# Kernel tuning notes

Hardware: AMD Instinct MI355X
Metric: run time of the kernel (lower is better)

Reference implementation:

```python
import jax, jax.numpy as jnp
import numpy as np

N_NODES = 200000
N_EDGES = 3200000
N_FEAT = 128
N_GRAPHS = 1000
N_CLASSES = 10
K = 30          # sort-pool k
C_CAT = 97      # 32+32+32+1 concatenated channels


def _glorot(k, shape):
    fan = shape[0] + shape[-1]
    return jax.random.normal(k, shape, jnp.float32) * (2.0 / fan) ** 0.5


def setup_inputs() -> dict:
    key = jax.random.key(0)
    ks = jax.random.split(key, 20)
    x = jax.random.normal(ks[0], (N_NODES, N_FEAT), jnp.float32)
    edge_index = jax.random.randint(ks[1], (2, N_EDGES), 0, N_NODES, jnp.int32)
    batch = jnp.sort(jax.random.randint(ks[2], (N_NODES,), 0, N_GRAPHS, jnp.int32))
    params = dict(
        W1=_glorot(ks[3], (N_FEAT, 32)), b1=jnp.zeros((32,), jnp.float32),
        W2=_glorot(ks[4], (32, 32)),     b2=jnp.zeros((32,), jnp.float32),
        W3=_glorot(ks[5], (32, 32)),     b3=jnp.zeros((32,), jnp.float32),
        W4=_glorot(ks[6], (32, 1)),      b4=jnp.zeros((1,), jnp.float32),
        conv5_w=_glorot(ks[7], (16, 1, 97)),  conv5_b=jnp.zeros((16,), jnp.float32),
        conv6_w=_glorot(ks[8], (32, 16, 5)),  conv6_b=jnp.zeros((32,), jnp.float32),
        fc1_w=_glorot(ks[9], (352, 128)),     fc1_b=jnp.zeros((128,), jnp.float32),
        fc2_w=_glorot(ks[10], (128, N_CLASSES)), fc2_b=jnp.zeros((N_CLASSES,), jnp.float32),
    )
    return dict(x=x, edge_index=edge_index, batch=batch, **params)


def reference(x, edge_index, batch, W1, b1, W2, b2, W3, b3, W4, b4,
              conv5_w, conv5_b, conv6_w, conv6_b, fc1_w, fc1_b, fc2_w, fc2_b):
    N = x.shape[0]
    src, dst = edge_index[0], edge_index[1]
    emask = (src != dst).astype(x.dtype)            # remove_self_loops
    deg = jax.ops.segment_sum(emask, dst, num_segments=N) + 1.0  # +1 for added self-loop
    inv_sqrt = jax.lax.rsqrt(deg)
    coef = emask * inv_sqrt[src] * inv_sqrt[dst]    # D^-1/2 (A) D^-1/2 edge weight
    inv_deg = 1.0 / deg                             # self-loop weight

    def gcn(h, W, b):
        hw = h @ W
        agg = jax.ops.segment_sum(hw[src] * coef[:, None], dst, num_segments=N)
        return agg + hw * inv_deg[:, None] + b

    x1 = jnp.tanh(gcn(x, W1, b1))
    x2 = jnp.tanh(gcn(x1, W2, b2))
    x3 = jnp.tanh(gcn(x2, W3, b3))
    x4 = jnp.tanh(gcn(x3, W4, b4))
    xc = jnp.concatenate([x1, x2, x3, x4], axis=-1)  # [N, 97]

    # SortAggregation(k=30): per-graph descending sort by last channel, top-k, zero pad
    perm = jnp.lexsort((-xc[:, -1], batch))          # batch-major, last channel desc
    xs, bs = xc[perm], batch[perm]
    counts = jax.ops.segment_sum(jnp.ones_like(batch), batch, num_segments=N_GRAPHS)
    starts = jnp.cumsum(counts) - counts
    rank = jnp.arange(N, dtype=jnp.int32) - starts[bs]
    valid = rank < K
    pooled = jnp.zeros((N_GRAPHS, K, C_CAT), xc.dtype).at[
        bs, jnp.where(valid, rank, K - 1)].add(jnp.where(valid[:, None], xs, 0.0))

    z = pooled.reshape(N_GRAPHS, 1, K * C_CAT)       # [G, 1, 2910]
    dn = ('NCH', 'OIH', 'NCH')
    z = jax.lax.conv_general_dilated(z, conv5_w, (97,), 'VALID', dimension_numbers=dn)
    z = jax.nn.relu(z + conv5_b[None, :, None])      # [G, 16, 30]
    z = jax.lax.reduce_window(z, -jnp.inf, jax.lax.max, (1, 1, 2), (1, 1, 2), 'VALID')
    z = jax.lax.conv_general_dilated(z, conv6_w, (1,), 'VALID', dimension_numbers=dn)
    z = jax.nn.relu(z + conv6_b[None, :, None])      # [G, 32, 11]
    z = z.reshape(N_GRAPHS, -1)                      # [G, 352]
    h = jax.nn.relu(z @ fc1_w + fc1_b)               # dropout is identity in eval
    return jax.nn.log_softmax(h @ fc2_w + fc2_b, axis=-1)
```

## Files before the change

kernel.cpp:

```cpp
#include <hip/hip_runtime.h>
#include <math.h>

#define NN 200000
#define NE 3200000
#define NF 128
#define NG 1000
#define KSEL 30
#define CCAT 97
#define NPAD 200704
#define SCAN_BLKS 196
#define EPADCAP (NE + 8 * NN)

#define BWID 512
#define NB 391
#define BCAP 10240
#define P1_CHUNK 8192
#define P1_BLKS 391

__global__ void k_p1_partition(const int* __restrict__ ei, int* __restrict__ bcursor,
                               int* __restrict__ ebuf) {
    __shared__ int lhist[NB];
    __shared__ int lbase[NB];
    int tid = threadIdx.x;
    int base = blockIdx.x * P1_CHUNK;
    for (int b = tid; b < NB; b += 256) lhist[b] = 0;
    __syncthreads();
    for (int it = 0; it < P1_CHUNK / 256; it++) {
        int e = base + it * 256 + tid;
        if (e < NE) {
            int s = ei[e], d = ei[NE + e];
            if (s != d) atomicAdd(&lhist[d >> 9], 1);
        }
    }
    __syncthreads();
    for (int b = tid; b < NB; b += 256) {
        int cnt = lhist[b];
        lbase[b] = cnt ? atomicAdd(&bcursor[b], cnt) : 0;
        lhist[b] = 0;
    }
    __syncthreads();
    for (int it = 0; it < P1_CHUNK / 256; it++) {
        int e = base + it * 256 + tid;
        if (e < NE) {
            int s = ei[e], d = ei[NE + e];
            if (s != d) {
                int b = d >> 9;
                int r = atomicAdd(&lhist[b], 1);
                int pos = lbase[b] + r;
                if (pos >= BCAP) pos = BCAP - 1;
                ebuf[b * BCAP + pos] = s | ((d & 511) << 18);
            }
        }
    }
}

__global__ void k_p2_count(const int* __restrict__ bcursor, const int* __restrict__ ebuf,
                           int* __restrict__ rowcnt, float* __restrict__ inv_sqrt) {
    __shared__ int lcnt[BWID];
    int b = blockIdx.x;
    int tid = threadIdx.x;
    for (int i = tid; i < BWID; i += 256) lcnt[i] = 0;
    __syncthreads();
    int size = bcursor[b];
    if (size > BCAP) size = BCAP;
    const int* eb = ebuf + b * BCAP;
    for (int k = tid; k < size; k += 256) atomicAdd(&lcnt[eb[k] >> 18], 1);
    __syncthreads();
    int node0 = b * BWID;
    for (int i = tid; i < BWID; i += 256) {
        int node = node0 + i;
        if (node < NN) {
            int c = lcnt[i];
            rowcnt[node] = (c + 7) & ~7;
            inv_sqrt[node] = rsqrtf((float)(c + 1));
        }
    }
}

__global__ void k_scanA(const int* __restrict__ in, int* __restrict__ out,
                        int* __restrict__ bsums) {
    __shared__ int s[1024];
    int tid = threadIdx.x;
    int gid = blockIdx.x * 1024 + tid;
    int v = in[gid];
    s[tid] = v;
    __syncthreads();
    for (int off = 1; off < 1024; off <<= 1) {
        int a = (tid >= off) ? s[tid - off] : 0;
        int cur = s[tid];
        __syncthreads();
        s[tid] = cur + a;
        __syncthreads();
    }
    out[gid] = s[tid] - v;
    if (tid == 1023) bsums[blockIdx.x] = s[tid];
}

__global__ void k_scanB(int* __restrict__ bsums) {
    __shared__ int s[256];
    int tid = threadIdx.x;
    int v = (tid < SCAN_BLKS) ? bsums[tid] : 0;
    s[tid] = v;
    __syncthreads();
    for (int off = 1; off < 256; off <<= 1) {
        int a = (tid >= off) ? s[tid - off] : 0;
        int cur = s[tid];
        __syncthreads();
        s[tid] = cur + a;
        __syncthreads();
    }
    if (tid < SCAN_BLKS) bsums[tid] = s[tid] - v;
}

__global__ void k_scanC(int* __restrict__ out, const int* __restrict__ bsums) {
    int gid = blockIdx.x * 1024 + threadIdx.x;
    out[gid] += bsums[blockIdx.x];
}

__global__ void k_p3_scatter(const int* __restrict__ bcursor, const int* __restrict__ ebuf,
                             const int* __restrict__ rowstart, int* __restrict__ esrc) {
    __shared__ int lcur[BWID];
    int b = blockIdx.x;
    int tid = threadIdx.x;
    int node0 = b * BWID;
    for (int i = tid; i < BWID; i += 256) lcur[i] = rowstart[node0 + i];
    __syncthreads();
    int size = bcursor[b];
    if (size > BCAP) size = BCAP;
    const int* eb = ebuf + b * BCAP;
    for (int k = tid; k < size; k += 256) {
        int v = eb[k];
        int local = v >> 18;
        int pos = atomicAdd(&lcur[local], 1);
        esrc[pos] = v & 0x3FFFF;
    }
    __syncthreads();
    for (int i = tid; i < BWID; i += 256) {
        int node = node0 + i;
        if (node < NN) {
            int end = rowstart[node + 1];
            for (int p = lcur[i]; p < end; p++) esrc[p] = NN;
        }
    }
}

template <int K>
__global__ void __launch_bounds__(256, 3) k_mm(const float* __restrict__ X,
                                               const float* __restrict__ W,
                                               const float* __restrict__ inv_sqrt,
                                               float* __restrict__ Y) {
    constexpr int K4 = K / 4;
    constexpr int RS = K4 + 1;
    __shared__ float4 sW[K * 8];
    __shared__ float4 sX[64 * RS];
    int tid = threadIdx.x;
    for (int i = tid; i < K * 8; i += 256) sW[i] = ((const float4*)W)[i];
    const float4* __restrict__ Xg = (const float4*)(X + (size_t)blockIdx.x * 64 * K);
    for (int i = tid; i < 64 * K4; i += 256) {
        int row = i / K4;
        int col = i & (K4 - 1);
        sX[row * RS + col] = Xg[i];
    }
    __syncthreads();
    int g = tid >> 3;
    int q = tid & 7;
    int r0 = blockIdx.x * 64 + g * 2;
    const float4* __restrict__ xr0 = &sX[(size_t)(g * 2 + 0) * RS];
    const float4* __restrict__ xr1 = &sX[(size_t)(g * 2 + 1) * RS];
    float4 a0 = make_float4(0.f, 0.f, 0.f, 0.f);
    float4 a1 = make_float4(0.f, 0.f, 0.f, 0.f);
#pragma unroll 4
    for (int k4 = 0; k4 < K4; k4++) {
        float4 x0 = xr0[k4];
        float4 x1 = xr1[k4];
        const float4* wk = &sW[k4 * 32 + q];
#pragma unroll
        for (int kk = 0; kk < 4; kk++) {
            float4 w = wk[kk * 8];
            float s0 = (kk == 0) ? x0.x : (kk == 1) ? x0.y : (kk == 2) ? x0.z : x0.w;
            float s1 = (kk == 0) ? x1.x : (kk == 1) ? x1.y : (kk == 2) ? x1.z : x1.w;
            a0.x = fmaf(s0, w.x, a0.x); a0.y = fmaf(s0, w.y, a0.y);
            a0.z = fmaf(s0, w.z, a0.z); a0.w = fmaf(s0, w.w, a0.w);
            a1.x = fmaf(s1, w.x, a1.x); a1.y = fmaf(s1, w.y, a1.y);
            a1.z = fmaf(s1, w.z, a1.z); a1.w = fmaf(s1, w.w, a1.w);
        }
    }
    float s0 = inv_sqrt[r0 + 0];
    float s1 = inv_sqrt[r0 + 1];
    a0.x *= s0; a0.y *= s0; a0.z *= s0; a0.w *= s0;
    a1.x *= s1; a1.y *= s1; a1.z *= s1; a1.w *= s1;
    ((float4*)(Y + (size_t)(r0 + 0) * 32))[q] = a0;
    ((float4*)(Y + (size_t)(r0 + 1) * 32))[q] = a1;
}

__global__ void k_aggr(const int* __restrict__ rowstart, const int* __restrict__ esrc,
                       const float* __restrict__ hws, const float* __restrict__ inv_sqrt,
                       const float* __restrict__ b, float* __restrict__ xout) {
    int t = blockIdx.x * 256 + threadIdx.x;
    int n = t >> 5, c = t & 31;
    if (n >= NN) return;
    int e0 = rowstart[n], e1 = rowstart[n + 1];
    float a[8];
    a[0] = hws[(size_t)n * 32 + c];
#pragma unroll
    for (int k = 1; k < 8; k++) a[k] = 0.0f;
    for (int e = e0; e < e1; e += 8) {
        int4 sA = *(const int4*)(esrc + e);
        int4 sB = *(const int4*)(esrc + e + 4);
        float v0 = hws[(size_t)sA.x * 32 + c];
        float v1 = hws[(size_t)sA.y * 32 + c];
        float v2 = hws[(size_t)sA.z * 32 + c];
        float v3 = hws[(size_t)sA.w * 32 + c];
        float v4 = hws[(size_t)sB.x * 32 + c];
        float v5 = hws[(size_t)sB.y * 32 + c];
        float v6 = hws[(size_t)sB.z * 32 + c];
        float v7 = hws[(size_t)sB.w * 32 + c];
        a[0] += v0; a[1] += v1; a[2] += v2; a[3] += v3;
        a[4] += v4; a[5] += v5; a[6] += v6; a[7] += v7;
    }
    float acc = ((a[0] + a[1]) + (a[2] + a[3])) + ((a[4] + a[5]) + (a[6] + a[7]));
    xout[t] = tanhf(fmaf(acc, inv_sqrt[n], b[c]));
}

__global__ void k_mm4(const float* __restrict__ x3, const float* __restrict__ W4,
                      const float* __restrict__ inv_sqrt, float* __restrict__ hws4) {
    int n = blockIdx.x * 256 + threadIdx.x;
    if (n >= NN) return;
    if (n == 0) hws4[NN] = 0.0f;
    const float4* xr = (const float4*)(x3 + (size_t)n * 32);
    float acc = 0.0f;
#pragma unroll
    for (int q = 0; q < 8; q++) {
        float4 v = xr[q];
        acc = fmaf(v.x, W4[q * 4 + 0], acc);
        acc = fmaf(v.y, W4[q * 4 + 1], acc);
        acc = fmaf(v.z, W4[q * 4 + 2], acc);
        acc = fmaf(v.w, W4[q * 4 + 3], acc);
    }
    hws4[n] = acc * inv_sqrt[n];
}

__global__ void k_aggr1(const int* __restrict__ rowstart, const int* __restrict__ esrc,
                        const float* __restrict__ hws4, const float* __restrict__ inv_sqrt,
                        const float* __restrict__ b4, float* __restrict__ x4) {
    int n = blockIdx.x * 256 + threadIdx.x;
    if (n >= NN) return;
    int e0 = rowstart[n], e1 = rowstart[n + 1];
    float a[8];
    a[0] = hws4[n];
#pragma unroll
    for (int k = 1; k < 8; k++) a[k] = 0.0f;
    for (int e = e0; e < e1; e += 8) {
        int4 sA = *(const int4*)(esrc + e);
        int4 sB = *(const int4*)(esrc + e + 4);
        a[0] += hws4[sA.x]; a[1] += hws4[sA.y];
        a[2] += hws4[sA.z]; a[3] += hws4[sA.w];
        a[4] += hws4[sB.x]; a[5] += hws4[sB.y];
        a[6] += hws4[sB.z]; a[7] += hws4[sB.w];
    }
    float acc = ((a[0] + a[1]) + (a[2] + a[3])) + ((a[4] + a[5]) + (a[6] + a[7]));
    x4[n] = tanhf(fmaf(acc, inv_sqrt[n], b4[0]));
}

__global__ void k_gbounds(const int* __restrict__ batch, int* __restrict__ starts) {
    int n = blockIdx.x * 256 + threadIdx.x;
    if (n >= NN) return;
    int bn = batch[n];
    int bp = (n == 0) ? -1 : batch[n - 1];
    for (int g = bp + 1; g <= bn; g++) starts[g] = n;
    if (n == NN - 1)
        for (int g = bn + 1; g <= NG; g++) starts[g] = NN;
}

__global__ void k_sortpool(const int* __restrict__ starts,
                           const float* __restrict__ x1, const float* __restrict__ x2,
                           const float* __restrict__ x3, const float* __restrict__ x4,
                           float* __restrict__ pooled) {
    __shared__ float keys[1024];
    __shared__ int sel[KSEL];
    int g = blockIdx.x;
    int tid = threadIdx.x;
    int start = starts[g];
    int cnt = starts[g + 1] - start;
    if (cnt > 1024) cnt = 1024;
    for (int i = tid; i < cnt; i += 256) keys[i] = x4[start + i];
    __syncthreads();
    for (int i = tid; i < cnt; i += 256) {
        float ki = keys[i];
        int rank = 0;
        for (int j = 0; j < cnt; j++) {
            float kj = keys[j];
            rank += (kj > ki) || (kj == ki && j < i);
        }
        if (rank < KSEL) sel[rank] = start + i;
    }
    __syncthreads();
    int selcnt = cnt < KSEL ? cnt : KSEL;
    for (int t = tid; t < KSEL * CCAT; t += 256) {
        int r = t / CCAT, ch = t - r * CCAT;
        float v = 0.0f;
        if (r < selcnt) {
            int node = sel[r];
            if (ch < 32)      v = x1[(size_t)node * 32 + ch];
            else if (ch < 64) v = x2[(size_t)node * 32 + ch - 32];
            else if (ch < 96) v = x3[(size_t)node * 32 + ch - 64];
            else              v = x4[node];
        }
        pooled[g * (KSEL * CCAT) + t] = v;
    }
}

__global__ void k_head(const float* __restrict__ pooled,
                       const float* __restrict__ w5, const float* __restrict__ b5,
                       const float* __restrict__ w6, const float* __restrict__ b6,
                       const float* __restrict__ fw1, const float* __restrict__ fb1,
                       const float* __restrict__ fw2, const float* __restrict__ fb2,
                       float* __restrict__ out) {
    __shared__ float sP[KSEL * CCAT];
    __shared__ float s5[16 * 30];
    __shared__ float smp[16 * 15];
    __shared__ float sz[352];
    __shared__ float sh[128];
    __shared__ float sl[10];
    int g = blockIdx.x;
    int tid = threadIdx.x;
    for (int i = tid; i < KSEL * CCAT; i += 256) sP[i] = pooled[g * (KSEL * CCAT) + i];
    __syncthreads();
    for (int t = tid; t < 16 * 30; t += 256) {
        int c = t / 30, j = t - c * 30;
        float acc = b5[c];
        for (int i = 0; i < CCAT; i++) acc = fmaf(sP[j * CCAT + i], w5[c * CCAT + i], acc);
        s5[c * 30 + j] = fmaxf(acc, 0.0f);
    }
    __syncthreads();
    for (int t = tid; t < 16 * 15; t += 256) {
        int c = t / 15, j = t - c * 15;
        smp[t] = fmaxf(s5[c * 30 + 2 * j], s5[c * 30 + 2 * j + 1]);
    }
    __syncthreads();
    for (int t = tid; t < 32 * 11; t += 256) {
        int c = t / 11, j = t - c * 11;
        float acc = b6[c];
        for (int ci = 0; ci < 16; ci++) {
#pragma unroll
            for (int k = 0; k < 5; k++)
                acc = fmaf(smp[ci * 15 + j + k], w6[(c * 16 + ci) * 5 + k], acc);
        }
        sz[t] = fmaxf(acc, 0.0f);
    }
    __syncthreads();
    if (tid < 128) {
        float acc = fb1[tid];
        for (int i = 0; i < 352; i++) acc = fmaf(sz[i], fw1[i * 128 + tid], acc);
        sh[tid] = fmaxf(acc, 0.0f);
    }
    __syncthreads();
    if (tid < 10) {
        float acc = fb2[tid];
        for (int i = 0; i < 128; i++) acc = fmaf(sh[i], fw2[i * 10 + tid], acc);
        sl[tid] = acc;
    }
    __syncthreads();
    if (tid < 10) {
        float m = -1e30f;
        for (int i = 0; i < 10; i++) m = fmaxf(m, sl[i]);
        float ssum = 0.0f;
        for (int i = 0; i < 10; i++) ssum += expf(sl[i] - m);
        out[g * 10 + tid] = sl[tid] - m - logf(ssum);
    }
}

extern "C" void kernel_launch(void* const* d_in, const int* in_sizes, int n_in,
                              void* d_out, int out_size, void* d_ws, size_t ws_size,
                              hipStream_t stream) {
    const float* x   = (const float*)d_in[0];
    const int*   ei  = (const int*)d_in[1];
    const int*   bat = (const int*)d_in[2];
    const float* W1  = (const float*)d_in[3];
    const float* b1  = (const float*)d_in[4];
    const float* W2  = (const float*)d_in[5];
    const float* b2  = (const float*)d_in[6];
    const float* W3  = (const float*)d_in[7];
    const float* b3  = (const float*)d_in[8];
    const float* W4  = (const float*)d_in[9];
    const float* b4  = (const float*)d_in[10];
    const float* w5  = (const float*)d_in[11];
    const float* b5  = (const float*)d_in[12];
    const float* w6  = (const float*)d_in[13];
    const float* b6  = (const float*)d_in[14];
    const float* fw1 = (const float*)d_in[15];
    const float* fb1 = (const float*)d_in[16];
    const float* fw2 = (const float*)d_in[17];
    const float* fb2 = (const float*)d_in[18];
    float* out = (float*)d_out;

    float* ws = (float*)d_ws;
    float* inv_sqrt = ws;
    float* hws      = inv_sqrt + NN;
    float* x1       = hws + (size_t)(NN + 1) * 32;
    float* x2       = x1 + (size_t)NN * 32;
    float* x3       = x2 + (size_t)NN * 32;
    float* x4       = x3 + (size_t)NN * 32;
    float* pooled   = x4 + NN;
    int* rowcnt     = (int*)(pooled + NG * KSEL * CCAT);
    int* rowstart   = rowcnt + NPAD;
    int* esrc       = rowstart + NPAD;
    int* bcursor    = esrc + EPADCAP;
    int* bsums      = bcursor + 512;
    int* gstarts    = bsums + 256;
    int* ebuf       = (int*)x3;

    const int TB = 256;
    int gN  = (NN + TB - 1) / TB;
    int gNC = (NN * 32 + TB - 1) / TB;
    int gMM = NN / 64;

    hipMemsetAsync(bcursor, 0, 512 * sizeof(int), stream);
    hipMemsetAsync(rowcnt, 0, NPAD * sizeof(int), stream);
    hipMemsetAsync(hws + (size_t)NN * 32, 0, 32 * sizeof(float), stream);
    k_p1_partition<<<P1_BLKS, TB, 0, stream>>>(ei, bcursor, ebuf);
    k_p2_count<<<NB, TB, 0, stream>>>(bcursor, ebuf, rowcnt, inv_sqrt);
    k_scanA<<<SCAN_BLKS, 1024, 0, stream>>>(rowcnt, rowstart, bsums);
    k_scanB<<<1, 256, 0, stream>>>(bsums);
    k_scanC<<<SCAN_BLKS, 1024, 0, stream>>>(rowstart, bsums);
    k_p3_scatter<<<NB, TB, 0, stream>>>(bcursor, ebuf, rowstart, esrc);

    k_gbounds<<<gN, TB, 0, stream>>>(bat, gstarts);

    k_mm<128><<<gMM, TB, 0, stream>>>(x, W1, inv_sqrt, hws);
    k_aggr<<<gNC, TB, 0, stream>>>(rowstart, esrc, hws, inv_sqrt, b1, x1);
    k_mm<32><<<gMM, TB, 0, stream>>>(x1, W2, inv_sqrt, hws);
    k_aggr<<<gNC, TB, 0, stream>>>(rowstart, esrc, hws, inv_sqrt, b2, x2);
    k_mm<32><<<gMM, TB, 0, stream>>>(x2, W3, inv_sqrt, hws);
    k_aggr<<<gNC, TB, 0, stream>>>(rowstart, esrc, hws, inv_sqrt, b3, x3);
    k_mm4<<<gN, TB, 0, stream>>>(x3, W4, inv_sqrt, hws);
    k_aggr1<<<gN, TB, 0, stream>>>(rowstart, esrc, hws, inv_sqrt, b4, x4);

    k_sortpool<<<NG, TB, 0, stream>>>(gstarts, x1, x2, x3, x4, pooled);
    k_head<<<NG, TB, 0, stream>>>(pooled, w5, b5, w6, b6, fw1, fb1, fw2, fb2, out);
}
```

Before: 585.6 us.

## Fuse next-layer matmul into aggregation epilogue and merge sortpool with head

The GCN aggregation kernel now computes the next layer's dense projection (32x32 or 32x1) in its epilogue, using shared memory for the row and a warp-shuffle reduction for the single-column case. Ping-pong hws buffers remove the separate k_mm and k_mm4 launches and their re-reads of x1/x2/x3. Sort-pool and the conv/FC head are merged into one kernel so the pooled tensor stays in shared memory instead of going through global memory. In exchange, each aggregation thread holds a 32-float weight column, which raises register pressure, and the aggregation kernel gains a block barrier.

```diff
diff --git a/kernel.cpp b/kernel.cpp
--- a/kernel.cpp
+++ b/kernel.cpp
@@ -193,12 +193,14 @@
     ((float4*)(Y + (size_t)(r0 + 1) * 32))[q] = a1;
 }
 
-__global__ void k_aggr(const int* __restrict__ rowstart, const int* __restrict__ esrc,
-                       const float* __restrict__ hws, const float* __restrict__ inv_sqrt,
-                       const float* __restrict__ b, float* __restrict__ xout) {
+template <int MODE>
+__global__ void k_aggr_f(const int* __restrict__ rowstart, const int* __restrict__ esrc,
+                         const float* __restrict__ hws, const float* __restrict__ inv_sqrt,
+                         const float* __restrict__ bvec, const float* __restrict__ Wn,
+                         float* __restrict__ xout, float* __restrict__ hnext) {
+    __shared__ float sxr[8][32];
     int t = blockIdx.x * 256 + threadIdx.x;
     int n = t >> 5, c = t & 31;
-    if (n >= NN) return;
     int e0 = rowstart[n], e1 = rowstart[n + 1];
     float a[8];
     a[0] = hws[(size_t)n * 32 + c];
@@ -219,25 +221,37 @@
         a[4] += v4; a[5] += v5; a[6] += v6; a[7] += v7;
     }
     float acc = ((a[0] + a[1]) + (a[2] + a[3])) + ((a[4] + a[5]) + (a[6] + a[7]));
-    xout[t] = tanhf(fmaf(acc, inv_sqrt[n], b[c]));
-}
-
-__global__ void k_mm4(const float* __restrict__ x3, const float* __restrict__ W4,
-                      const float* __restrict__ inv_sqrt, float* __restrict__ hws4) {
-    int n = blockIdx.x * 256 + threadIdx.x;
-    if (n >= NN) return;
-    if (n == 0) hws4[NN] = 0.0f;
-    const float4* xr = (const float4*)(x3 + (size_t)n * 32);
-    float acc = 0.0f;
-#pragma unroll
-    for (int q = 0; q < 8; q++) {
-        float4 v = xr[q];
-        acc = fmaf(v.x, W4[q * 4 + 0], acc);
-        acc = fmaf(v.y, W4[q * 4 + 1], acc);
-        acc = fmaf(v.z, W4[q * 4 + 2], acc);
-        acc = fmaf(v.w, W4[q * 4 + 3], acc);
-    }
-    hws4[n] = acc * inv_sqrt[n];
+    float invs = inv_sqrt[n];
+    float r = tanhf(fmaf(acc, invs, bvec[c]));
+    xout[t] = r;
+    if (MODE == 1) {
+        int ln = threadIdx.x >> 5;
+        sxr[ln][c] = r;
+        float wcol[32];
+#pragma unroll
+        for (int k = 0; k < 32; k++) wcol[k] = Wn[k * 32 + c];
+        __syncthreads();
+        const float4* xr = (const float4*)sxr[ln];
+        float h = 0.f;
+#pragma unroll
+        for (int j = 0; j < 8; j++) {
+            float4 xq = xr[j];
+            h = fmaf(xq.x, wcol[4 * j + 0], h);
+            h = fmaf(xq.y, wcol[4 * j + 1], h);
+            h = fmaf(xq.z, wcol[4 * j + 2], h);
+            h = fmaf(xq.w, wcol[4 * j + 3], h);
+        }
+        hnext[t] = h * invs;
+    } else {
+        float v = r * Wn[c];
+        v += __shfl_xor(v, 1);
+        v += __shfl_xor(v, 2);
+        v += __shfl_xor(v, 4);
+        v += __shfl_xor(v, 8);
+        v += __shfl_xor(v, 16);
+        if (c == 0) hnext[n] = v * invs;
+        if (t == 0) hnext[NN] = 0.f;
+    }
 }
 
 __global__ void k_aggr1(const int* __restrict__ rowstart, const int* __restrict__ esrc,
@@ -272,12 +286,22 @@
         for (int g = bn + 1; g <= NG; g++) starts[g] = NN;
 }
 
-__global__ void k_sortpool(const int* __restrict__ starts,
-                           const float* __restrict__ x1, const float* __restrict__ x2,
-                           const float* __restrict__ x3, const float* __restrict__ x4,
-                           float* __restrict__ pooled) {
+__global__ void k_tail(const int* __restrict__ starts,
+                       const float* __restrict__ x1, const float* __restrict__ x2,
+                       const float* __restrict__ x3, const float* __restrict__ x4,
+                       const float* __restrict__ w5, const float* __restrict__ b5,
+                       const float* __restrict__ w6, const float* __restrict__ b6,
+                       const float* __restrict__ fw1, const float* __restrict__ fb1,
+                       const float* __restrict__ fw2, const float* __restrict__ fb2,
+                       float* __restrict__ out) {
     __shared__ float keys[1024];
     __shared__ int sel[KSEL];
+    __shared__ float sP[KSEL * CCAT];
+    __shared__ float s5[16 * 30];
+    __shared__ float smp[16 * 15];
+    __shared__ float sz[352];
+    __shared__ float sh[128];
+    __shared__ float sl[10];
     int g = blockIdx.x;
     int tid = threadIdx.x;
     int start = starts[g];
@@ -306,25 +330,8 @@
             else if (ch < 96) v = x3[(size_t)node * 32 + ch - 64];
             else              v = x4[node];
         }
-        pooled[g * (KSEL * CCAT) + t] = v;
-    }
-}
-
-__global__ void k_head(const float* __restrict__ pooled,
-                       const float* __restrict__ w5, const float* __restrict__ b5,
-                       const float* __restrict__ w6, const float* __restrict__ b6,
-                       const float* __restrict__ fw1, const float* __restrict__ fb1,
-                       const float* __restrict__ fw2, const float* __restrict__ fb2,
-                       float* __restrict__ out) {
-    __shared__ float sP[KSEL * CCAT];
-    __shared__ float s5[16 * 30];
-    __shared__ float smp[16 * 15];
-    __shared__ float sz[352];
-    __shared__ float sh[128];
-    __shared__ float sl[10];
-    int g = blockIdx.x;
-    int tid = threadIdx.x;
-    for (int i = tid; i < KSEL * CCAT; i += 256) sP[i] = pooled[g * (KSEL * CCAT) + i];
+        sP[t] = v;
+    }
     __syncthreads();
     for (int t = tid; t < 16 * 30; t += 256) {
         int c = t / 30, j = t - c * 30;
@@ -396,13 +403,13 @@
 
     float* ws = (float*)d_ws;
     float* inv_sqrt = ws;
-    float* hws      = inv_sqrt + NN;
-    float* x1       = hws + (size_t)(NN + 1) * 32;
+    float* hwsA     = inv_sqrt + NN;
+    float* hwsB     = hwsA + (size_t)(NN + 1) * 32;
+    float* x1       = hwsB + (size_t)(NN + 1) * 32;
     float* x2       = x1 + (size_t)NN * 32;
     float* x3       = x2 + (size_t)NN * 32;
     float* x4       = x3 + (size_t)NN * 32;
-    float* pooled   = x4 + NN;
-    int* rowcnt     = (int*)(pooled + NG * KSEL * CCAT);
+    int* rowcnt     = (int*)(x4 + NN);
     int* rowstart   = rowcnt + NPAD;
     int* esrc       = rowstart + NPAD;
     int* bcursor    = esrc + EPADCAP;
@@ -412,12 +419,13 @@
 
     const int TB = 256;
     int gN  = (NN + TB - 1) / TB;
-    int gNC = (NN * 32 + TB - 1) / TB;
+    int gNC = (NN * 32) / TB;
     int gMM = NN / 64;
 
     hipMemsetAsync(bcursor, 0, 512 * sizeof(int), stream);
     hipMemsetAsync(rowcnt, 0, NPAD * sizeof(int), stream);
-    hipMemsetAsync(hws + (size_t)NN * 32, 0, 32 * sizeof(float), stream);
+    hipMemsetAsync(hwsA + (size_t)NN * 32, 0, 32 * sizeof(float), stream);
+    hipMemsetAsync(hwsB + (size_t)NN * 32, 0, 32 * sizeof(float), stream);
     k_p1_partition<<<P1_BLKS, TB, 0, stream>>>(ei, bcursor, ebuf);
     k_p2_count<<<NB, TB, 0, stream>>>(bcursor, ebuf, rowcnt, inv_sqrt);
     k_scanA<<<SCAN_BLKS, 1024, 0, stream>>>(rowcnt, rowstart, bsums);
@@ -427,15 +435,12 @@
 
     k_gbounds<<<gN, TB, 0, stream>>>(bat, gstarts);
 
-    k_mm<128><<<gMM, TB, 0, stream>>>(x, W1, inv_sqrt, hws);
-    k_aggr<<<gNC, TB, 0, stream>>>(rowstart, esrc, hws, inv_sqrt, b1, x1);
-    k_mm<32><<<gMM, TB, 0, stream>>>(x1, W2, inv_sqrt, hws);
-    k_aggr<<<gNC, TB, 0, stream>>>(rowstart, esrc, hws, inv_sqrt, b2, x2);
-    k_mm<32><<<gMM, TB, 0, stream>>>(x2, W3, inv_sqrt, hws);
-    k_aggr<<<gNC, TB, 0, stream>>>(rowstart, esrc, hws, inv_sqrt, b3, x3);
-    k_mm4<<<gN, TB, 0, stream>>>(x3, W4, inv_sqrt, hws);
-    k_aggr1<<<gN, TB, 0, stream>>>(rowstart, esrc, hws, inv_sqrt, b4, x4);
-
-    k_sortpool<<<NG, TB, 0, stream>>>(gstarts, x1, x2, x3, x4, pooled);
-    k_head<<<NG, TB, 0, stream>>>(pooled, w5, b5, w6, b6, fw1, fb1, fw2, fb2, out);
-}
+    k_mm<128><<<gMM, TB, 0, stream>>>(x, W1, inv_sqrt, hwsA);
+    k_aggr_f<1><<<gNC, TB, 0, stream>>>(rowstart, esrc, hwsA, inv_sqrt, b1, W2, x1, hwsB);
+    k_aggr_f<1><<<gNC, TB, 0, stream>>>(rowstart, esrc, hwsB, inv_sqrt, b2, W3, x2, hwsA);
+    k_aggr_f<2><<<gNC, TB, 0, stream>>>(rowstart, esrc, hwsA, inv_sqrt, b3, W4, x3, hwsB);
+    k_aggr1<<<gN, TB, 0, stream>>>(rowstart, esrc, hwsB, inv_sqrt, b4, x4);
+
+    k_tail<<<NG, TB, 0, stream>>>(gstarts, x1, x2, x3, x4,
+                                  w5, b5, w6, b6, fw1, fb1, fw2, fb2, out);
+}
```

New measurement: 575.1 us. No clear change (-1.8%).
